# Kernel tuning notes

Measured on AMD Instinct MI355X. Metric: run time of the kernel, lower is better.

The kernel has to match this reference:

```python
import jax, jax.numpy as jnp
import numpy as np

N = 100000
E = 1600000
D_IN = 128
H1 = 128
H2 = 128
C = 64


def setup_inputs() -> dict:
    key = jax.random.key(0)
    ks = jax.random.split(key, 10)
    x_content = jax.random.normal(ks[0], (N, D_IN), dtype=jnp.float32)
    edge_index = jax.random.randint(ks[1], (2, E), 0, N, dtype=jnp.int64)
    # SAGEConv params: lin_l (applied to aggregated neighbors, has bias),
    # lin_r (applied to root node, no bias). Kaiming-ish scaling.
    def lin(k, fan_in, fan_out):
        return jax.random.normal(k, (fan_in, fan_out), dtype=jnp.float32) / np.sqrt(fan_in)
    return {
        "x_content": x_content,
        "edge_index": edge_index,
        "W1l": lin(ks[2], D_IN, H1),
        "b1": jnp.zeros((H1,), jnp.float32),
        "W1r": lin(ks[3], D_IN, H1),
        "W2l": lin(ks[4], H1, H2),
        "b2": jnp.zeros((H2,), jnp.float32),
        "W2r": lin(ks[5], H1, H2),
        "Wout": lin(ks[6], H2, C),
        "bout": jnp.zeros((C,), jnp.float32),
    }


def _sage_conv(x, src, dst, Wl, b, Wr):
    # mean-aggregate neighbor features (messages flow src -> dst), then
    # out = mean_agg @ Wl + b + x @ Wr  (PyG SAGEConv, aggr='mean')
    msgs = x[src]                                            # [E, d]
    agg = jax.ops.segment_sum(msgs, dst, num_segments=N)     # [N, d]
    deg = jax.ops.segment_sum(jnp.ones((src.shape[0],), x.dtype), dst, num_segments=N)
    mean = agg / jnp.clip(deg, 1.0)[:, None]
    return mean @ Wl + b + x @ Wr


def reference(x_content, edge_index, W1l, b1, W1r, W2l, b2, W2r, Wout, bout):
    src, dst = edge_index[0], edge_index[1]
    # dropout is identity in eval mode (training=False)
    x = jax.nn.relu(_sage_conv(x_content, src, dst, W1l, b1, W1r))
    x = jax.nn.relu(_sage_conv(x, src, dst, W2l, b2, W2r))
    return x @ Wout + bout
```

## Files before the change

### kernel.cpp

```cpp
#include <hip/hip_runtime.h>

#define DD 128
#define CC 64
#define BKW 512
#define NPB 4096

typedef __attribute__((ext_vector_type(8))) short short8v;
typedef __attribute__((ext_vector_type(4))) float f32x4;
typedef __attribute__((ext_vector_type(2))) float f32x2;

static __device__ inline ushort f2bf_rne(float f) {
    unsigned u = __float_as_uint(f);
    unsigned r = (u + 0x7FFFu + ((u >> 16) & 1u)) >> 16;
    return (ushort)r;
}
static __device__ inline float bf2f(ushort h) {
    return __uint_as_float(((unsigned)h) << 16);
}
static __device__ inline float bflo(uint u) {
    return __uint_as_float(u << 16);
}
static __device__ inline float bfhi(uint u) {
    return __uint_as_float(u & 0xffff0000u);
}

__global__ __launch_bounds__(256) void bucket_cnt_kernel(const int* __restrict__ ei,
                                                         int* __restrict__ bcnt, int E) {
    __shared__ int h[256];
    const int t = threadIdx.x;
    h[t] = 0;
    __syncthreads();
    const int base = blockIdx.x * 8192;
    const int end = min(E, base + 8192);
    for (int j = base + t; j < end; j += 256) {
        atomicAdd(&h[ei[E + j] >> 9], 1);
    }
    __syncthreads();
    if (h[t]) atomicAdd(&bcnt[t], h[t]);
}

__global__ __launch_bounds__(256) void bucket_scan_kernel(const int* __restrict__ bcnt,
                                                          int* __restrict__ boffs,
                                                          int* __restrict__ bcur) {
    __shared__ int s[256];
    const int t = threadIdx.x;
    int v = bcnt[t];
    s[t] = v;
    __syncthreads();
    for (int off = 1; off < 256; off <<= 1) {
        int xv = 0;
        if (t >= off) xv = s[t - off];
        __syncthreads();
        if (t >= off) s[t] += xv;
        __syncthreads();
    }
    int excl = s[t] - v;
    boffs[t] = excl;
    bcur[t] = excl;
    if (t == 255) boffs[256] = s[255];
}

__global__ __launch_bounds__(256) void binA_kernel(const int* __restrict__ ei,
                                                   int* __restrict__ bcur,
                                                   uint* __restrict__ ebuf, int E) {
    __shared__ int sRun[256];
    __shared__ int sRel[256];
    __shared__ int sBase[256];
    __shared__ uint sPair[NPB];
    __shared__ unsigned char sBkt[NPB];
    __shared__ int sHist[256];
    const int t = threadIdx.x;
    const int e0 = blockIdx.x * NPB;
    const int cntE = min(NPB, E - e0);

    sHist[t] = 0;
    __syncthreads();
    for (int j = t; j < cntE; j += 256) {
        int dst = ei[E + e0 + j];
        atomicAdd(&sHist[dst >> 9], 1);
    }
    __syncthreads();
    int h = sHist[t];
    sRun[t] = h;
    __syncthreads();
    for (int off = 1; off < 256; off <<= 1) {
        int v = 0;
        if (t >= off) v = sRun[t - off];
        __syncthreads();
        if (t >= off) sRun[t] += v;
        __syncthreads();
    }
    int runstart = sRun[t] - h;
    int base = 0;
    if (h > 0) base = atomicAdd(&bcur[t], h);
    sRun[t] = runstart;
    sRel[t] = runstart;
    sBase[t] = base;
    __syncthreads();
    for (int j = t; j < cntE; j += 256) {
        int src = ei[e0 + j];
        int dst = ei[E + e0 + j];
        int b = dst >> 9;
        int slot = atomicAdd(&sRel[b], 1);
        sPair[slot] = (uint)src | ((uint)(dst & 511) << 17);
        sBkt[slot] = (unsigned char)b;
    }
    __syncthreads();
    for (int s = t; s < cntE; s += 256) {
        uint p = sPair[s];
        int b = (int)sBkt[s];
        int gpos = sBase[b] + (s - sRun[b]);
        ebuf[gpos] = p;
    }
}

__global__ __launch_bounds__(256) void binB2_kernel(const uint* __restrict__ ebuf,
                                                    const int* __restrict__ boffs,
                                                    int* __restrict__ offs,
                                                    int* __restrict__ cnt,
                                                    int* __restrict__ csr, int n) {
    __shared__ int sCnt[BKW];
    __shared__ int sOffs[BKW];
    __shared__ int sScan[256];
    const int t = threadIdx.x;
    const int node0 = blockIdx.x * BKW;
    const int start = boffs[blockIdx.x];
    const int end = boffs[blockIdx.x + 1];

    sCnt[t] = 0; sCnt[t + 256] = 0;
    __syncthreads();
    for (int j = start + t; j < end; j += 256) {
        int d = (int)(ebuf[j] >> 17);
        atomicAdd(&sCnt[d], 1);
    }
    __syncthreads();
    int v0 = sCnt[2 * t], v1 = sCnt[2 * t + 1];
    int sum = v0 + v1;
    sScan[t] = sum;
    __syncthreads();
    for (int off = 1; off < 256; off <<= 1) {
        int xv = 0;
        if (t >= off) xv = sScan[t - off];
        __syncthreads();
        if (t >= off) sScan[t] += xv;
        __syncthreads();
    }
    int excl = sScan[t] - sum;
    sOffs[2 * t] = start + excl;
    sOffs[2 * t + 1] = start + excl + v0;
    __syncthreads();
    for (int i = t; i < BKW; i += 256) {
        int node = node0 + i;
        if (node < n) { offs[node] = sOffs[i]; cnt[node] = sCnt[i]; }
    }
    __syncthreads();
    sCnt[t] = 0; sCnt[t + 256] = 0;
    __syncthreads();
    for (int j = start + t; j < end; j += 256) {
        uint p = ebuf[j];
        int d = (int)(p >> 17);
        int r = atomicAdd(&sCnt[d], 1);
        csr[sOffs[d] + r] = (int)(p & 0x1FFFFu);
    }
}

__global__ __launch_bounds__(256) void xsplit_kernel(const float* __restrict__ x,
                                                     ushort* __restrict__ xh,
                                                     int total8) {
    int i = blockIdx.x * 256 + threadIdx.x;
    if (i >= total8) return;
    float4 a = ((const float4*)x)[2 * i];
    float4 b = ((const float4*)x)[2 * i + 1];
    ushort r[8] = {f2bf_rne(a.x), f2bf_rne(a.y), f2bf_rne(a.z), f2bf_rne(a.w),
                   f2bf_rne(b.x), f2bf_rne(b.y), f2bf_rne(b.z), f2bf_rne(b.w)};
    uint4 o;
    o.x = (uint)r[0] | ((uint)r[1] << 16);
    o.y = (uint)r[2] | ((uint)r[3] << 16);
    o.z = (uint)r[4] | ((uint)r[5] << 16);
    o.w = (uint)r[6] | ((uint)r[7] << 16);
    ((uint4*)xh)[i] = o;
}

__global__ __launch_bounds__(256) void csr_agg4_kernel(
    const ushort* __restrict__ xh, const int* __restrict__ offs,
    const int* __restrict__ cnt, const int* __restrict__ csr,
    ushort* __restrict__ meanH, int n) {
    int node = blockIdx.x * 4 + (threadIdx.x >> 6);
    if (node >= n) return;
    const int lane = threadIdx.x & 63;
    const int sub = lane >> 4;
    const int li = lane & 15;
    const int start = offs[node];
    const int c = cnt[node];
    f32x2 a[4], aa[4];
    #pragma unroll
    for (int k = 0; k < 4; ++k) { a[k] = (f32x2){0.f, 0.f}; aa[k] = (f32x2){0.f, 0.f}; }
    #define ACC4(A, U) \
        A[0] += (f32x2){bflo(U.x), bfhi(U.x)}; \
        A[1] += (f32x2){bflo(U.y), bfhi(U.y)}; \
        A[2] += (f32x2){bflo(U.z), bfhi(U.z)}; \
        A[3] += (f32x2){bflo(U.w), bfhi(U.w)};
    const int c16 = c & ~15;
    int j = 0;
    if (c16 > 0) {
        int s0 = csr[start + sub];
        int s1 = csr[start + 4 + sub];
        int s2 = csr[start + 8 + sub];
        int s3 = csr[start + 12 + sub];
        for (; j < c16; j += 16) {
            int t0 = 0, t1 = 0, t2 = 0, t3 = 0;
            if (j + 16 < c16) {
                t0 = csr[start + j + 16 + sub];
                t1 = csr[start + j + 20 + sub];
                t2 = csr[start + j + 24 + sub];
                t3 = csr[start + j + 28 + sub];
            }
            uint4 u0 = *(const uint4*)(xh + (size_t)s0 * DD + li * 8);
            uint4 u1 = *(const uint4*)(xh + (size_t)s1 * DD + li * 8);
            uint4 u2 = *(const uint4*)(xh + (size_t)s2 * DD + li * 8);
            uint4 u3 = *(const uint4*)(xh + (size_t)s3 * DD + li * 8);
            ACC4(a, u0); ACC4(a, u1); ACC4(aa, u2); ACC4(aa, u3);
            s0 = t0; s1 = t1; s2 = t2; s3 = t3;
        }
    }
    if (c - j >= 8) {
        int s0 = csr[start + j + sub];
        int s1 = csr[start + j + 4 + sub];
        uint4 u0 = *(const uint4*)(xh + (size_t)s0 * DD + li * 8);
        uint4 u1 = *(const uint4*)(xh + (size_t)s1 * DD + li * 8);
        ACC4(a, u0); ACC4(aa, u1);
        j += 8;
    }
    if (c - j >= 4) {
        int s = csr[start + j + sub];
        uint4 u = *(const uint4*)(xh + (size_t)s * DD + li * 8);
        ACC4(a, u);
        j += 4;
    }
    if (j + sub < c) {
        int s = csr[start + j + sub];
        uint4 u = *(const uint4*)(xh + (size_t)s * DD + li * 8);
        ACC4(aa, u);
    }
    #undef ACC4
    float res[8];
    #pragma unroll
    for (int k = 0; k < 4; ++k) {
        f32x2 v = a[k] + aa[k];
        float e0 = v.x; e0 += __shfl_xor(e0, 16); e0 += __shfl_xor(e0, 32);
        float e1 = v.y; e1 += __shfl_xor(e1, 16); e1 += __shfl_xor(e1, 32);
        res[2 * k] = e0; res[2 * k + 1] = e1;
    }
    if (sub == 0) {
        float inv = 1.0f / fmaxf((float)c, 1.0f);
        short8v o;
        #pragma unroll
        for (int k = 0; k < 8; ++k) o[k] = (short)f2bf_rne(res[k] * inv);
        *(short8v*)(meanH + (size_t)node * DD + li * 8) = o;
    }
}

__global__ __launch_bounds__(256) void wfrag_kernel(
    const float* __restrict__ Wl1, const float* __restrict__ Wr1,
    const float* __restrict__ Wl2, const float* __restrict__ Wr2,
    ushort* __restrict__ WTfrag1, ushort* __restrict__ WTfrag2) {
    int idx = blockIdx.x * 256 + threadIdx.x;
    if (idx >= 4096) return;
    const float* Wl = blockIdx.y ? Wl2 : Wl1;
    const float* Wr = blockIdx.y ? Wr2 : Wr1;
    ushort* dst = (blockIdx.y ? WTfrag2 : WTfrag1) + (size_t)idx * 8;
    int lane = idx & 63, t = (idx >> 6) & 7, s = idx >> 9;
    int col = t * 16 + (lane & 15);
    int k0 = s * 32 + (lane >> 4) * 8;
    #pragma unroll
    for (int j = 0; j < 8; ++j) {
        int k = k0 + j;
        float v = (k < DD) ? Wl[k * DD + col] : Wr[(k - DD) * DD + col];
        dst[j] = f2bf_rne(v);
    }
}

__global__ __launch_bounds__(256) void wofrag_kernel(const float* __restrict__ Wout,
                                                     ushort* __restrict__ WoFrag) {
    int idx = blockIdx.x * 256 + threadIdx.x;
    if (idx >= 1024) return;
    ushort* dst = WoFrag + (size_t)idx * 8;
    int lane = idx & 63, t = (idx >> 6) & 3, kc = idx >> 8;
    int col = t * 16 + (lane & 15);
    int k0 = kc * 32 + (lane >> 4) * 8;
    #pragma unroll
    for (int j = 0; j < 8; ++j) {
        dst[j] = f2bf_rne(Wout[(k0 + j) * CC + col]);
    }
}

template <bool PROJ>
__global__ __launch_bounds__(512) void layer_mfma_kernel(
    const ushort* __restrict__ meanH, const ushort* __restrict__ rootH,
    const ushort* __restrict__ WTfrag, const float* __restrict__ bias,
    ushort* __restrict__ outH,
    const ushort* __restrict__ WoFrag, const float* __restrict__ bout,
    float* __restrict__ outF, int n) {
    __shared__ ushort sB[32768];
    const int tid = threadIdx.x;
    const int w = tid >> 6;
    const int l = tid & 63;
    const int row0 = blockIdx.x * 128;
    const int lrow = w * 16 + (l & 15);
    const int kb = (l >> 4) * 8;
    const int lcol = l & 15;
    const int arowg = min(row0 + lrow, n - 1);

    const ushort* Am = meanH + (size_t)arowg * DD;
    const ushort* Ar = rootH + (size_t)arowg * DD;

    short8v ap[8];
    #pragma unroll
    for (int s = 0; s < 8; ++s) {
        ap[s] = (s < 4) ? *(const short8v*)(Am + s * 32 + kb)
                        : *(const short8v*)(Ar + (s - 4) * 32 + kb);
    }
    for (int i = tid; i < 4096; i += 512) {
        ((short8v*)sB)[i] = ((const short8v*)WTfrag)[i];
    }
    __syncthreads();

    f32x4 acc[8];
    #pragma unroll
    for (int t = 0; t < 8; ++t) acc[t] = (f32x4){0.f, 0.f, 0.f, 0.f};

    #pragma unroll
    for (int s = 0; s < 8; ++s) {
        #pragma unroll
        for (int t = 0; t < 8; ++t) {
            short8v bh = *(const short8v*)&sB[s * 4096 + t * 512 + l * 8];
            acc[t] = __builtin_amdgcn_mfma_f32_16x16x32_bf16(ap[s], bh, acc[t], 0, 0, 0);
        }
    }

    const int lrow0 = w * 16 + (l >> 4) * 4;
    if (!PROJ) {
        #pragma unroll
        for (int t = 0; t < 8; ++t) {
            const int col = t * 16 + lcol;
            const float b = bias[col];
            #pragma unroll
            for (int r = 0; r < 4; ++r) {
                int row = row0 + lrow0 + r;
                if (row < n)
                    outH[(size_t)row * DD + col] = f2bf_rne(fmaxf(acc[t][r] + b, 0.f));
            }
        }
    } else {
        __syncthreads();
        ushort (*sH)[136] = (ushort(*)[136])sB;
        #pragma unroll
        for (int t = 0; t < 8; ++t) {
            const int col = t * 16 + lcol;
            const float b = bias[col];
            #pragma unroll
            for (int r = 0; r < 4; ++r) {
                sH[lrow0 + r][col] = f2bf_rne(fmaxf(acc[t][r] + b, 0.f));
            }
        }
        f32x4 po[4];
        #pragma unroll
        for (int t = 0; t < 4; ++t) po[t] = (f32x4){0.f, 0.f, 0.f, 0.f};
        #pragma unroll
        for (int kc = 0; kc < 4; ++kc) {
            short8v ah = *(const short8v*)&sH[lrow][kc * 32 + kb];
            const ushort* fb = WoFrag + (size_t)kc * 2048 + l * 8;
            #pragma unroll
            for (int t = 0; t < 4; ++t) {
                short8v bh = *(const short8v*)(fb + t * 512);
                po[t] = __builtin_amdgcn_mfma_f32_16x16x32_bf16(ah, bh, po[t], 0, 0, 0);
            }
        }
        #pragma unroll
        for (int t = 0; t < 4; ++t) {
            const int col = t * 16 + lcol;
            const float b = bout[col];
            #pragma unroll
            for (int r = 0; r < 4; ++r) {
                int row = row0 + lrow0 + r;
                if (row < n) outF[(size_t)row * CC + col] = po[t][r] + b;
            }
        }
    }
}

extern "C" void kernel_launch(void* const* d_in, const int* in_sizes, int n_in,
                              void* d_out, int out_size, void* d_ws, size_t ws_size,
                              hipStream_t stream) {
    const float* x    = (const float*)d_in[0];
    const int*   ei   = (const int*)d_in[1];
    const float* W1l  = (const float*)d_in[2];
    const float* b1   = (const float*)d_in[3];
    const float* W1r  = (const float*)d_in[4];
    const float* W2l  = (const float*)d_in[5];
    const float* b2   = (const float*)d_in[6];
    const float* W2r  = (const float*)d_in[7];
    const float* Wout = (const float*)d_in[8];
    const float* bout = (const float*)d_in[9];
    float* out = (float*)d_out;
    const int n = in_sizes[0] / DD;
    const int E = in_sizes[1] / 2;
    const size_t NP = (size_t)n * DD;

    const int NBUCK = (n + BKW - 1) / BKW;

    int* cnt   = (int*)d_ws;
    int* offs  = cnt + 100352;
    int* bcnt  = offs + 100352;
    int* boffs = bcnt + 256;
    int* bcur  = boffs + 512;
    int* csr   = bcur + 256;
    uint* ebuf = (uint*)(csr + 1600256);
    ushort* xh  = (ushort*)ebuf;
    ushort* meanH = xh + NP;
    ushort* h1h = meanH + NP;
    ushort* WTfrag1 = h1h + NP;
    ushort* WTfrag2 = WTfrag1 + 32768;
    ushort* WoFrag  = WTfrag2 + 32768;

    hipMemsetAsync(bcnt, 0, sizeof(int) * 256, stream);
    bucket_cnt_kernel<<<(E + 8191) / 8192, 256, 0, stream>>>(ei, bcnt, E);
    bucket_scan_kernel<<<1, 256, 0, stream>>>(bcnt, boffs, bcur);
    binA_kernel<<<(E + NPB - 1) / NPB, 256, 0, stream>>>(ei, bcur, ebuf, E);
    binB2_kernel<<<NBUCK, 256, 0, stream>>>(ebuf, boffs, offs, cnt, csr, n);

    dim3 wgrid(16, 2);
    wfrag_kernel<<<wgrid, 256, 0, stream>>>(W1l, W1r, W2l, W2r, WTfrag1, WTfrag2);
    wofrag_kernel<<<4, 256, 0, stream>>>(Wout, WoFrag);

    xsplit_kernel<<<(n * DD / 8 + 255) / 256, 256, 0, stream>>>(x, xh, n * DD / 8);

    const int nblk = (n + 127) / 128;
    const int ablk = (n + 3) / 4;

    csr_agg4_kernel<<<ablk, 256, 0, stream>>>(xh, offs, cnt, csr, meanH, n);
    layer_mfma_kernel<false><<<nblk, 512, 0, stream>>>(
        meanH, xh, WTfrag1, b1, h1h,
        (const ushort*)nullptr, (const float*)nullptr, (float*)nullptr, n);

    csr_agg4_kernel<<<ablk, 256, 0, stream>>>(h1h, offs, cnt, csr, meanH, n);
    layer_mfma_kernel<true><<<nblk, 512, 0, stream>>>(
        meanH, h1h, WTfrag2, b2, (ushort*)nullptr,
        WoFrag, bout, out, n);
}
```

Baseline: 250.4 us.

## Gather layer-1 neighbor features in fp8 and fuse prep kernels

Measured after the change: 233.7 us. -6.7%, faster.

```diff
diff --git a/kernel.cpp b/kernel.cpp
--- a/kernel.cpp
+++ b/kernel.cpp
@@ -1,4 +1,5 @@
 #include <hip/hip_runtime.h>
+#include <hip/hip_fp8.h>
 
 #define DD 128
 #define CC 64
@@ -117,13 +118,13 @@
 __global__ __launch_bounds__(256) void binB2_kernel(const uint* __restrict__ ebuf,
                                                     const int* __restrict__ boffs,
                                                     int* __restrict__ offs,
-                                                    int* __restrict__ cnt,
                                                     int* __restrict__ csr, int n) {
     __shared__ int sCnt[BKW];
     __shared__ int sOffs[BKW];
     __shared__ int sScan[256];
     const int t = threadIdx.x;
     const int node0 = blockIdx.x * BKW;
+    const int node1 = min(n, node0 + BKW);
     const int start = boffs[blockIdx.x];
     const int end = boffs[blockIdx.x + 1];
 
@@ -151,8 +152,9 @@
     __syncthreads();
     for (int i = t; i < BKW; i += 256) {
         int node = node0 + i;
-        if (node < n) { offs[node] = sOffs[i]; cnt[node] = sCnt[i]; }
-    }
+        if (node < n) offs[node] = sOffs[i];
+    }
+    if (node1 == n && t == 0) offs[n] = end;
     __syncthreads();
     sCnt[t] = 0; sCnt[t + 256] = 0;
     __syncthreads();
@@ -164,34 +166,154 @@
     }
 }
 
-__global__ __launch_bounds__(256) void xsplit_kernel(const float* __restrict__ x,
-                                                     ushort* __restrict__ xh,
-                                                     int total8) {
-    int i = blockIdx.x * 256 + threadIdx.x;
-    if (i >= total8) return;
-    float4 a = ((const float4*)x)[2 * i];
-    float4 b = ((const float4*)x)[2 * i + 1];
-    ushort r[8] = {f2bf_rne(a.x), f2bf_rne(a.y), f2bf_rne(a.z), f2bf_rne(a.w),
-                   f2bf_rne(b.x), f2bf_rne(b.y), f2bf_rne(b.z), f2bf_rne(b.w)};
-    uint4 o;
-    o.x = (uint)r[0] | ((uint)r[1] << 16);
-    o.y = (uint)r[2] | ((uint)r[3] << 16);
-    o.z = (uint)r[4] | ((uint)r[5] << 16);
-    o.w = (uint)r[6] | ((uint)r[7] << 16);
-    ((uint4*)xh)[i] = o;
-}
-
-__global__ __launch_bounds__(256) void csr_agg4_kernel(
-    const ushort* __restrict__ xh, const int* __restrict__ offs,
-    const int* __restrict__ cnt, const int* __restrict__ csr,
-    ushort* __restrict__ meanH, int n) {
+__global__ __launch_bounds__(256) void prep_kernel(
+    const float* __restrict__ x, ushort* __restrict__ xh, uint* __restrict__ xq,
+    const float* __restrict__ Wl1, const float* __restrict__ Wr1,
+    const float* __restrict__ Wl2, const float* __restrict__ Wr2,
+    const float* __restrict__ Wout,
+    ushort* __restrict__ WTfrag1, ushort* __restrict__ WTfrag2,
+    ushort* __restrict__ WoFrag, int nxblk) {
+    const int t = threadIdx.x;
+    const int bx = blockIdx.x;
+    if (bx < nxblk) {
+        int i = bx * 256 + t;
+        float4 a = ((const float4*)x)[2 * i];
+        float4 b = ((const float4*)x)[2 * i + 1];
+        float vv[8] = {a.x, a.y, a.z, a.w, b.x, b.y, b.z, b.w};
+        ushort r[8];
+        uint q[8];
+        #pragma unroll
+        for (int j = 0; j < 8; ++j) {
+            r[j] = f2bf_rne(vv[j]);
+            q[j] = (uint)__hip_fp8_e4m3(vv[j]).__x;
+        }
+        uint4 o;
+        o.x = (uint)r[0] | ((uint)r[1] << 16);
+        o.y = (uint)r[2] | ((uint)r[3] << 16);
+        o.z = (uint)r[4] | ((uint)r[5] << 16);
+        o.w = (uint)r[6] | ((uint)r[7] << 16);
+        ((uint4*)xh)[i] = o;
+        uint2 oq;
+        oq.x = q[0] | (q[1] << 8) | (q[2] << 16) | (q[3] << 24);
+        oq.y = q[4] | (q[5] << 8) | (q[6] << 16) | (q[7] << 24);
+        ((uint2*)xq)[i] = oq;
+    } else if (bx < nxblk + 32) {
+        int li = bx - nxblk;
+        int layer = li >> 4;
+        int idx = (li & 15) * 256 + t;
+        const float* Wl = layer ? Wl2 : Wl1;
+        const float* Wr = layer ? Wr2 : Wr1;
+        ushort* dst = (layer ? WTfrag2 : WTfrag1) + (size_t)idx * 8;
+        int lane = idx & 63, tt = (idx >> 6) & 7, s = idx >> 9;
+        int col = tt * 16 + (lane & 15);
+        int k0 = s * 32 + (lane >> 4) * 8;
+        #pragma unroll
+        for (int j = 0; j < 8; ++j) {
+            int k = k0 + j;
+            float v = (k < DD) ? Wl[k * DD + col] : Wr[(k - DD) * DD + col];
+            dst[j] = f2bf_rne(v);
+        }
+    } else {
+        int idx = (bx - nxblk - 32) * 256 + t;
+        ushort* dst = WoFrag + (size_t)idx * 8;
+        int lane = idx & 63, tt = (idx >> 6) & 3, kc = idx >> 8;
+        int col = tt * 16 + (lane & 15);
+        int k0 = kc * 32 + (lane >> 4) * 8;
+        #pragma unroll
+        for (int j = 0; j < 8; ++j) {
+            dst[j] = f2bf_rne(Wout[(k0 + j) * CC + col]);
+        }
+    }
+}
+
+__global__ __launch_bounds__(256) void csr_agg8_kernel(
+    const uint* __restrict__ xq, const int* __restrict__ offs,
+    const int* __restrict__ csr, ushort* __restrict__ meanH, int n) {
     int node = blockIdx.x * 4 + (threadIdx.x >> 6);
     if (node >= n) return;
     const int lane = threadIdx.x & 63;
     const int sub = lane >> 4;
     const int li = lane & 15;
     const int start = offs[node];
-    const int c = cnt[node];
+    const int c = offs[node + 1] - start;
+    f32x2 a[4], aa[4];
+    #pragma unroll
+    for (int k = 0; k < 4; ++k) { a[k] = (f32x2){0.f, 0.f}; aa[k] = (f32x2){0.f, 0.f}; }
+    #define ACC8(A, U) { \
+        A[0] += __builtin_amdgcn_cvt_pk_f32_fp8(U.x, false); \
+        A[1] += __builtin_amdgcn_cvt_pk_f32_fp8(U.x, true);  \
+        A[2] += __builtin_amdgcn_cvt_pk_f32_fp8(U.y, false); \
+        A[3] += __builtin_amdgcn_cvt_pk_f32_fp8(U.y, true);  }
+    const int c16 = c & ~15;
+    int j = 0;
+    if (c16 > 0) {
+        int s0 = csr[start + sub];
+        int s1 = csr[start + 4 + sub];
+        int s2 = csr[start + 8 + sub];
+        int s3 = csr[start + 12 + sub];
+        for (; j < c16; j += 16) {
+            int t0 = 0, t1 = 0, t2 = 0, t3 = 0;
+            if (j + 16 < c16) {
+                t0 = csr[start + j + 16 + sub];
+                t1 = csr[start + j + 20 + sub];
+                t2 = csr[start + j + 24 + sub];
+                t3 = csr[start + j + 28 + sub];
+            }
+            uint2 u0 = *(const uint2*)((const uchar*)xq + (size_t)s0 * DD + li * 8);
+            uint2 u1 = *(const uint2*)((const uchar*)xq + (size_t)s1 * DD + li * 8);
+            uint2 u2 = *(const uint2*)((const uchar*)xq + (size_t)s2 * DD + li * 8);
+            uint2 u3 = *(const uint2*)((const uchar*)xq + (size_t)s3 * DD + li * 8);
+            ACC8(a, u0); ACC8(a, u1); ACC8(aa, u2); ACC8(aa, u3);
+            s0 = t0; s1 = t1; s2 = t2; s3 = t3;
+        }
+    }
+    if (c - j >= 8) {
+        int s0 = csr[start + j + sub];
+        int s1 = csr[start + j + 4 + sub];
+        uint2 u0 = *(const uint2*)((const uchar*)xq + (size_t)s0 * DD + li * 8);
+        uint2 u1 = *(const uint2*)((const uchar*)xq + (size_t)s1 * DD + li * 8);
+        ACC8(a, u0); ACC8(aa, u1);
+        j += 8;
+    }
+    if (c - j >= 4) {
+        int s = csr[start + j + sub];
+        uint2 u = *(const uint2*)((const uchar*)xq + (size_t)s * DD + li * 8);
+        ACC8(a, u);
+        j += 4;
+    }
+    if (j + sub < c) {
+        int s = csr[start + j + sub];
+        uint2 u = *(const uint2*)((const uchar*)xq + (size_t)s * DD + li * 8);
+        ACC8(aa, u);
+    }
+    #undef ACC8
+    float res[8];
+    #pragma unroll
+    for (int k = 0; k < 4; ++k) {
+        f32x2 v = a[k] + aa[k];
+        float e0 = v.x; e0 += __shfl_xor(e0, 16); e0 += __shfl_xor(e0, 32);
+        float e1 = v.y; e1 += __shfl_xor(e1, 16); e1 += __shfl_xor(e1, 32);
+        res[2 * k] = e0; res[2 * k + 1] = e1;
+    }
+    if (sub == 0) {
+        float inv = 1.0f / fmaxf((float)c, 1.0f);
+        short8v o;
+        #pragma unroll
+        for (int k = 0; k < 8; ++k) o[k] = (short)f2bf_rne(res[k] * inv);
+        *(short8v*)(meanH + (size_t)node * DD + li * 8) = o;
+    }
+}
+
+__global__ __launch_bounds__(256) void csr_agg4_kernel(
+    const ushort* __restrict__ xh, const int* __restrict__ offs,
+    const int* __restrict__ csr, ushort* __restrict__ meanH, int n) {
+    int node = blockIdx.x * 4 + (threadIdx.x >> 6);
+    if (node >= n) return;
+    const int lane = threadIdx.x & 63;
+    const int sub = lane >> 4;
+    const int li = lane & 15;
+    const int start = offs[node];
+    const int c = offs[node + 1] - start;
     f32x2 a[4], aa[4];
     #pragma unroll
     for (int k = 0; k < 4; ++k) { a[k] = (f32x2){0.f, 0.f}; aa[k] = (f32x2){0.f, 0.f}; }
@@ -260,40 +382,6 @@
     }
 }
 
-__global__ __launch_bounds__(256) void wfrag_kernel(
-    const float* __restrict__ Wl1, const float* __restrict__ Wr1,
-    const float* __restrict__ Wl2, const float* __restrict__ Wr2,
-    ushort* __restrict__ WTfrag1, ushort* __restrict__ WTfrag2) {
-    int idx = blockIdx.x * 256 + threadIdx.x;
-    if (idx >= 4096) return;
-    const float* Wl = blockIdx.y ? Wl2 : Wl1;
-    const float* Wr = blockIdx.y ? Wr2 : Wr1;
-    ushort* dst = (blockIdx.y ? WTfrag2 : WTfrag1) + (size_t)idx * 8;
-    int lane = idx & 63, t = (idx >> 6) & 7, s = idx >> 9;
-    int col = t * 16 + (lane & 15);
-    int k0 = s * 32 + (lane >> 4) * 8;
-    #pragma unroll
-    for (int j = 0; j < 8; ++j) {
-        int k = k0 + j;
-        float v = (k < DD) ? Wl[k * DD + col] : Wr[(k - DD) * DD + col];
-        dst[j] = f2bf_rne(v);
-    }
-}
-
-__global__ __launch_bounds__(256) void wofrag_kernel(const float* __restrict__ Wout,
-                                                     ushort* __restrict__ WoFrag) {
-    int idx = blockIdx.x * 256 + threadIdx.x;
-    if (idx >= 1024) return;
-    ushort* dst = WoFrag + (size_t)idx * 8;
-    int lane = idx & 63, t = (idx >> 6) & 3, kc = idx >> 8;
-    int col = t * 16 + (lane & 15);
-    int k0 = kc * 32 + (lane >> 4) * 8;
-    #pragma unroll
-    for (int j = 0; j < 8; ++j) {
-        dst[j] = f2bf_rne(Wout[(k0 + j) * CC + col]);
-    }
-}
-
 template <bool PROJ>
 __global__ __launch_bounds__(512) void layer_mfma_kernel(
     const ushort* __restrict__ meanH, const ushort* __restrict__ rootH,
@@ -409,14 +497,14 @@
 
     const int NBUCK = (n + BKW - 1) / BKW;
 
-    int* cnt   = (int*)d_ws;
-    int* offs  = cnt + 100352;
+    int* offs  = (int*)d_ws;
     int* bcnt  = offs + 100352;
     int* boffs = bcnt + 256;
     int* bcur  = boffs + 512;
     int* csr   = bcur + 256;
     uint* ebuf = (uint*)(csr + 1600256);
-    ushort* xh  = (ushort*)ebuf;
+    uint* xq   = ebuf;
+    ushort* xh = (ushort*)((uchar*)xq + NP);
     ushort* meanH = xh + NP;
     ushort* h1h = meanH + NP;
     ushort* WTfrag1 = h1h + NP;
@@ -427,23 +515,21 @@
     bucket_cnt_kernel<<<(E + 8191) / 8192, 256, 0, stream>>>(ei, bcnt, E);
     bucket_scan_kernel<<<1, 256, 0, stream>>>(bcnt, boffs, bcur);
     binA_kernel<<<(E + NPB - 1) / NPB, 256, 0, stream>>>(ei, bcur, ebuf, E);
-    binB2_kernel<<<NBUCK, 256, 0, stream>>>(ebuf, boffs, offs, cnt, csr, n);
-
-    dim3 wgrid(16, 2);
-    wfrag_kernel<<<wgrid, 256, 0, stream>>>(W1l, W1r, W2l, W2r, WTfrag1, WTfrag2);
-    wofrag_kernel<<<4, 256, 0, stream>>>(Wout, WoFrag);
-
-    xsplit_kernel<<<(n * DD / 8 + 255) / 256, 256, 0, stream>>>(x, xh, n * DD / 8);
+    binB2_kernel<<<NBUCK, 256, 0, stream>>>(ebuf, boffs, offs, csr, n);
+
+    const int nxblk = (int)(NP / 8 / 256);
+    prep_kernel<<<nxblk + 36, 256, 0, stream>>>(x, xh, xq, W1l, W1r, W2l, W2r,
+                                                Wout, WTfrag1, WTfrag2, WoFrag, nxblk);
 
     const int nblk = (n + 127) / 128;
     const int ablk = (n + 3) / 4;
 
-    csr_agg4_kernel<<<ablk, 256, 0, stream>>>(xh, offs, cnt, csr, meanH, n);
+    csr_agg8_kernel<<<ablk, 256, 0, stream>>>(xq, offs, csr, meanH, n);
     layer_mfma_kernel<false><<<nblk, 512, 0, stream>>>(
         meanH, xh, WTfrag1, b1, h1h,
         (const ushort*)nullptr, (const float*)nullptr, (float*)nullptr, n);
 
-    csr_agg4_kernel<<<ablk, 256, 0, stream>>>(h1h, offs, cnt, csr, meanH, n);
+    csr_agg4_kernel<<<ablk, 256, 0, stream>>>(h1h, offs, csr, meanH, n);
     layer_mfma_kernel<true><<<nblk, 512, 0, stream>>>(
         meanH, h1h, WTfrag2, b2, (ushort*)nullptr,
         WoFrag, bout, out, n);
```
